# Kernel optimization log

Measured on AMD Instinct MI355X. Metric: run time of the kernel, lower is better.

Reference implementation:

```python
import jax, jax.numpy as jnp
import numpy as np

EPS_NORM = 1e-12
EPS_ENT = 1e-12
TEMPERATURE = 0.5
CONTRAST_DENOM = 128.0 * 100.0


def _l2_normalize(x, axis=-1):
    n = jnp.linalg.norm(x, axis=axis, keepdims=True)
    return x / jnp.maximum(n, EPS_NORM)


def setup_inputs() -> dict:
    key0 = jax.random.key(0)
    k1, k2, k3, k4 = jax.random.split(key0, 4)
    B, L, C = 16, 2048, 512
    M = 512
    return {
        "key": jax.random.normal(k1, (B, L, C), dtype=jnp.float32),
        "query": jax.random.normal(k2, (B, L, C), dtype=jnp.float32),
        "keys": jax.random.uniform(k3, (M, C), dtype=jnp.float32),
        "values": jax.random.uniform(k4, (M, C), dtype=jnp.float32),
        "mode": 0,
    }


def reference(key, query, keys, values, mode):
    B, L, C = key.shape
    k = _l2_normalize(key.reshape(-1, C))    # [T, C]
    q = _l2_normalize(query.reshape(-1, C))  # [T, C]

    # --- gatheringLoss ---
    score = jnp.einsum('tc,mc->tm', k, keys)            # [T, M]
    # top-1 of softmax(score) == argmax(score) (softmax is monotone)
    idx = jnp.argmax(score, axis=1)                     # [T]
    nearest_values = values[idx]                        # [T, C]
    gathering_loss = jnp.mean((q - nearest_values) ** 2)

    logits = score / TEMPERATURE                        # [T, M]
    logp = jax.nn.log_softmax(logits, axis=-1)
    gathered = jnp.take_along_axis(logp, idx[:, None], axis=1)  # [T, 1]
    contrast_loss = jnp.sum(gathered) / (-CONTRAST_DENOM)

    # --- read ---
    weights = jax.nn.softmax(score, axis=-1)            # [T, M]
    # EntropyLoss: mean over rows of -sum(w * log(w + eps))
    entropy_loss = jnp.mean(-jnp.sum(weights * jnp.log(weights + EPS_ENT), axis=-1))
    read_query = weights @ values                       # [T, C]

    return (read_query.reshape(B, L, C), entropy_loss, gathering_loss,
            contrast_loss, keys, values)
```

## Files before the change

### kernel.cpp

```cpp
#include <hip/hip_runtime.h>

typedef short short8 __attribute__((ext_vector_type(8)));
typedef float floatx4 __attribute__((ext_vector_type(4)));

#define T_ROWS 32768
#define C_DIM 512
#define M_DIM 512

__device__ __forceinline__ unsigned short f2bf(float f) {
    unsigned u = __builtin_bit_cast(unsigned, f);
    u = u + 0x7fffu + ((u >> 16) & 1u);
    return (unsigned short)(u >> 16);
}

__global__ __launch_bounds__(256) void pack_kernel(
    const float* __restrict__ keys, const float* __restrict__ values,
    unsigned short* __restrict__ keysFrag, unsigned short* __restrict__ valsFrag) {
    int tid = blockIdx.x * 256 + threadIdx.x;
    int e  = tid & 32767;
    int l  = e & 63;
    int NT = (e >> 6) & 31;
    int kt = e >> 11;
    int li = l & 15, q4 = l >> 4;
    unsigned short tmp[8];
    if (tid < 32768) {
        const float* s = keys + (size_t)(NT * 16 + li) * C_DIM + kt * 32 + q4 * 8;
#pragma unroll
        for (int j = 0; j < 8; j++) tmp[j] = f2bf(s[j]);
        unsigned short* d = keysFrag + ((size_t)(kt * 32 + NT) * 64 + l) * 8;
        ushort4 a = make_ushort4(tmp[0], tmp[1], tmp[2], tmp[3]);
        ushort4 b = make_ushort4(tmp[4], tmp[5], tmp[6], tmp[7]);
        *(ushort4*)d = a;
        *(ushort4*)(d + 4) = b;
    } else {
#pragma unroll
        for (int j = 0; j < 8; j++)
            tmp[j] = f2bf(values[(size_t)(kt * 32 + q4 * 8 + j) * C_DIM + NT * 16 + li]);
        unsigned short* d = valsFrag + ((size_t)(kt * 32 + NT) * 64 + l) * 8;
        ushort4 a = make_ushort4(tmp[0], tmp[1], tmp[2], tmp[3]);
        ushort4 b = make_ushort4(tmp[4], tmp[5], tmp[6], tmp[7]);
        *(ushort4*)d = a;
        *(ushort4*)(d + 4) = b;
    }
}

__global__ __launch_bounds__(512) void fused_kernel(
    const float* __restrict__ key,
    const unsigned short* __restrict__ keysFrag,
    const unsigned short* __restrict__ valsFrag,
    float* __restrict__ outRQ,
    float* __restrict__ scal,
    int* __restrict__ idxOut) {
    __shared__ char kq[32 * 1040];
    __shared__ float stats[2][4][16][8];
    __shared__ float finals[32][2];

    const int tid = threadIdx.x;
    const int w  = tid >> 6;
    const int l  = tid & 63;
    const int li = l & 15;
    const int q4 = l >> 4;
    const int row0 = blockIdx.x << 5;

    {
        int r = (w << 2) + q4;
        const float4* src = (const float4*)(key + (size_t)(row0 + r) * C_DIM);
        float4 v[8];
        float ss = 0.f;
#pragma unroll
        for (int i = 0; i < 8; i++) {
            v[i] = src[i * 16 + li];
            ss += v[i].x * v[i].x + v[i].y * v[i].y + v[i].z * v[i].z + v[i].w * v[i].w;
        }
#pragma unroll
        for (int m = 1; m < 16; m <<= 1) ss += __shfl_xor(ss, m, 64);
        float inv = 1.0f / fmaxf(sqrtf(ss), 1e-12f);
        char* dstrow = kq + r * 1040;
#pragma unroll
        for (int i = 0; i < 8; i++) {
            ushort4 b = make_ushort4(f2bf(v[i].x * inv), f2bf(v[i].y * inv),
                                     f2bf(v[i].z * inv), f2bf(v[i].w * inv));
            *(ushort4*)(dstrow + i * 128 + li * 8) = b;
        }
    }
    __syncthreads();

    const int rg = w >> 2;
    const int mc = w & 3;
    floatx4 acc1[8];
#pragma unroll
    for (int i = 0; i < 8; i++) acc1[i] = (floatx4){0.f, 0.f, 0.f, 0.f};
    const short8* kf = (const short8*)keysFrag;
    for (int kt = 0; kt < 16; kt++) {
        short8 a = *(const short8*)(kq + (rg * 16 + li) * 1040 + kt * 64 + q4 * 16);
#pragma unroll
        for (int nt = 0; nt < 8; nt++) {
            short8 b = kf[(size_t)((kt * 32 + mc * 8 + nt) * 64 + l)];
            acc1[nt] = __builtin_amdgcn_mfma_f32_16x16x32_bf16(a, b, acc1[nt], 0, 0, 0);
        }
    }

#pragma unroll
    for (int reg = 0; reg < 4; reg++) {
        float m = acc1[0][reg];
        int bi = (mc * 8 + 0) * 16 + li;
#pragma unroll
        for (int nt = 1; nt < 8; nt++) {
            float s = acc1[nt][reg];
            if (s > m) { m = s; bi = (mc * 8 + nt) * 16 + li; }
        }
        float z1 = 0.f, e1 = 0.f, z2 = 0.f;
#pragma unroll
        for (int nt = 0; nt < 8; nt++) {
            float s = acc1[nt][reg];
            float p = __expf(s - m);
            z1 += p; e1 += p * s; z2 += p * p;
        }
#pragma unroll
        for (int msk = 1; msk < 16; msk <<= 1) {
            float mo  = __shfl_xor(m,  msk, 64);
            float z1o = __shfl_xor(z1, msk, 64);
            float e1o = __shfl_xor(e1, msk, 64);
            float z2o = __shfl_xor(z2, msk, 64);
            int   bio = __shfl_xor(bi, msk, 64);
            if (mo > m) {
                float sc = __expf(m - mo);
                z1 = z1 * sc + z1o; e1 = e1 * sc + e1o; z2 = z2 * sc * sc + z2o;
                m = mo; bi = bio;
            } else if (mo == m) {
                z1 += z1o; e1 += e1o; z2 += z2o; bi = min(bi, bio);
            } else {
                float sc = __expf(mo - m);
                z1 += z1o * sc; e1 += e1o * sc; z2 += z2o * sc * sc;
            }
        }
        if (li == 0) {
            float* st = stats[rg][mc][q4 * 4 + reg];
            st[0] = m; st[1] = z1; st[2] = e1; st[3] = z2;
            ((int*)st)[4] = bi;
        }
    }
    __syncthreads();

    if (tid < 32) {
        int r = tid;
        const float* st0 = stats[r >> 4][0][r & 15];
        float m = st0[0], z1 = st0[1], e1 = st0[2], z2 = st0[3];
        int bi = ((const int*)st0)[4];
#pragma unroll
        for (int p = 1; p < 4; p++) {
            const float* st = stats[r >> 4][p][r & 15];
            float mo = st[0], z1o = st[1], e1o = st[2], z2o = st[3];
            int bio = ((const int*)st)[4];
            if (mo > m) {
                float sc = __expf(m - mo);
                z1 = z1 * sc + z1o; e1 = e1 * sc + e1o; z2 = z2 * sc * sc + z2o;
                m = mo; bi = bio;
            } else if (mo == m) {
                z1 += z1o; e1 += e1o; z2 += z2o; bi = min(bi, bio);
            } else {
                float sc = __expf(mo - m);
                z1 += z1o * sc; e1 += e1o * sc; z2 += z2o * sc * sc;
            }
        }
        finals[r][0] = m;
        finals[r][1] = 1.0f / z1;
        idxOut[row0 + r] = bi;
        float ent = m + __logf(z1) - e1 / z1;
        float con = __logf(z2);
#pragma unroll
        for (int msk = 1; msk < 32; msk <<= 1) {
            ent += __shfl_xor(ent, msk, 64);
            con += __shfl_xor(con, msk, 64);
        }
        if (tid == 0) {
            atomicAdd(&scal[0], ent * (1.0f / 32768.0f));
            atomicAdd(&scal[2], con * (1.0f / 12800.0f));
        }
    }
    __syncthreads();

#pragma unroll
    for (int reg = 0; reg < 4; reg++) {
        int r = rg * 16 + q4 * 4 + reg;
        float m1 = finals[r][0];
#pragma unroll
        for (int nt = 0; nt < 8; nt++) {
            float p = __expf(acc1[nt][reg] - m1);
            int col = (mc * 8 + nt) * 16 + li;
            *(unsigned short*)(kq + r * 1040 + col * 2) = f2bf(p);
        }
    }
    __syncthreads();

    floatx4 acc2[2][4];
#pragma unroll
    for (int g = 0; g < 2; g++)
#pragma unroll
        for (int nt = 0; nt < 4; nt++) acc2[g][nt] = (floatx4){0.f, 0.f, 0.f, 0.f};
    const short8* vf = (const short8*)valsFrag;
    for (int kt = 0; kt < 16; kt++) {
        short8 a0 = *(const short8*)(kq + li * 1040 + kt * 64 + q4 * 16);
        short8 a1 = *(const short8*)(kq + (16 + li) * 1040 + kt * 64 + q4 * 16);
#pragma unroll
        for (int nt = 0; nt < 4; nt++) {
            short8 b = vf[(size_t)((kt * 32 + w * 4 + nt) * 64 + l)];
            acc2[0][nt] = __builtin_amdgcn_mfma_f32_16x16x32_bf16(a0, b, acc2[0][nt], 0, 0, 0);
            acc2[1][nt] = __builtin_amdgcn_mfma_f32_16x16x32_bf16(a1, b, acc2[1][nt], 0, 0, 0);
        }
    }

#pragma unroll
    for (int g = 0; g < 2; g++) {
#pragma unroll
        for (int reg = 0; reg < 4; reg++) {
            int r = g * 16 + q4 * 4 + reg;
            float iz = finals[r][1];
            float* orow = outRQ + (size_t)(row0 + r) * C_DIM + w * 64 + li;
#pragma unroll
            for (int nt = 0; nt < 4; nt++) orow[nt * 16] = acc2[g][nt][reg] * iz;
        }
    }
}

__global__ __launch_bounds__(256) void gather_kernel(
    const float* __restrict__ query, const float* __restrict__ values,
    const int* __restrict__ idx, float* __restrict__ slot) {
    __shared__ float red[4];
    const int tid = threadIdx.x, w = tid >> 6, l = tid & 63;
    float acc = 0.f;
#pragma unroll
    for (int rr = 0; rr < 8; rr++) {
        int t = (blockIdx.x << 5) + w * 8 + rr;
        const float4* qr = (const float4*)(query + (size_t)t * C_DIM);
        float4 a = qr[l * 2], b = qr[l * 2 + 1];
        float ss = a.x * a.x + a.y * a.y + a.z * a.z + a.w * a.w +
                   b.x * b.x + b.y * b.y + b.z * b.z + b.w * b.w;
#pragma unroll
        for (int m = 1; m < 64; m <<= 1) ss += __shfl_xor(ss, m, 64);
        float inv = 1.0f / fmaxf(sqrtf(ss), 1e-12f);
        const float4* vr = (const float4*)(values + (size_t)idx[t] * C_DIM);
        float4 va = vr[l * 2], vb = vr[l * 2 + 1];
        float d;
        d = a.x * inv - va.x; acc += d * d;
        d = a.y * inv - va.y; acc += d * d;
        d = a.z * inv - va.z; acc += d * d;
        d = a.w * inv - va.w; acc += d * d;
        d = b.x * inv - vb.x; acc += d * d;
        d = b.y * inv - vb.y; acc += d * d;
        d = b.z * inv - vb.z; acc += d * d;
        d = b.w * inv - vb.w; acc += d * d;
    }
#pragma unroll
    for (int m = 1; m < 64; m <<= 1) acc += __shfl_xor(acc, m, 64);
    if (l == 0) red[w] = acc;
    __syncthreads();
    if (tid == 0)
        atomicAdd(slot, (red[0] + red[1] + red[2] + red[3]) * (1.0f / (32768.0f * 512.0f)));
}

extern "C" void kernel_launch(void* const* d_in, const int* in_sizes, int n_in,
                              void* d_out, int out_size, void* d_ws, size_t ws_size,
                              hipStream_t stream) {
    (void)in_sizes; (void)n_in; (void)out_size; (void)ws_size;
    const float* key    = (const float*)d_in[0];
    const float* query  = (const float*)d_in[1];
    const float* keysIn = (const float*)d_in[2];
    const float* valsIn = (const float*)d_in[3];
    float* out = (float*)d_out;

    unsigned short* keysFrag = (unsigned short*)d_ws;
    unsigned short* valsFrag = keysFrag + 512 * 512;
    int* idxBuf = (int*)(valsFrag + 512 * 512);

    float* outRQ   = out;
    float* scal    = out + 16777216;
    float* keysOut = out + 16777219;
    float* valsOut = keysOut + 262144;

    hipMemsetAsync(scal, 0, 3 * sizeof(float), stream);
    hipMemcpyAsync(keysOut, keysIn, 262144 * sizeof(float), hipMemcpyDeviceToDevice, stream);
    hipMemcpyAsync(valsOut, valsIn, 262144 * sizeof(float), hipMemcpyDeviceToDevice, stream);

    pack_kernel<<<256, 256, 0, stream>>>(keysIn, valsIn, keysFrag, valsFrag);
    fused_kernel<<<1024, 512, 0, stream>>>(key, keysFrag, valsFrag, outRQ, scal, idxBuf);
    gather_kernel<<<1024, 256, 0, stream>>>(query, valsIn, idxBuf, scal + 1);
}
```

Measured before the change: 279.4 us.

## Process 64 rows per block, prefetch B fragments, fuse gather loss into main kernel

New measurement: 246.2 us. -11.9%, faster.

```diff
diff --git a/kernel.cpp b/kernel.cpp
--- a/kernel.cpp
+++ b/kernel.cpp
@@ -3,9 +3,8 @@
 typedef short short8 __attribute__((ext_vector_type(8)));
 typedef float floatx4 __attribute__((ext_vector_type(4)));
 
-#define T_ROWS 32768
 #define C_DIM 512
-#define M_DIM 512
+#define KQ_STRIDE 1040
 
 __device__ __forceinline__ unsigned short f2bf(float f) {
     unsigned u = __builtin_bit_cast(unsigned, f);
@@ -28,42 +27,42 @@
 #pragma unroll
         for (int j = 0; j < 8; j++) tmp[j] = f2bf(s[j]);
         unsigned short* d = keysFrag + ((size_t)(kt * 32 + NT) * 64 + l) * 8;
-        ushort4 a = make_ushort4(tmp[0], tmp[1], tmp[2], tmp[3]);
-        ushort4 b = make_ushort4(tmp[4], tmp[5], tmp[6], tmp[7]);
-        *(ushort4*)d = a;
-        *(ushort4*)(d + 4) = b;
+        *(ushort4*)d       = make_ushort4(tmp[0], tmp[1], tmp[2], tmp[3]);
+        *(ushort4*)(d + 4) = make_ushort4(tmp[4], tmp[5], tmp[6], tmp[7]);
     } else {
 #pragma unroll
         for (int j = 0; j < 8; j++)
             tmp[j] = f2bf(values[(size_t)(kt * 32 + q4 * 8 + j) * C_DIM + NT * 16 + li]);
         unsigned short* d = valsFrag + ((size_t)(kt * 32 + NT) * 64 + l) * 8;
-        ushort4 a = make_ushort4(tmp[0], tmp[1], tmp[2], tmp[3]);
-        ushort4 b = make_ushort4(tmp[4], tmp[5], tmp[6], tmp[7]);
-        *(ushort4*)d = a;
-        *(ushort4*)(d + 4) = b;
+        *(ushort4*)d       = make_ushort4(tmp[0], tmp[1], tmp[2], tmp[3]);
+        *(ushort4*)(d + 4) = make_ushort4(tmp[4], tmp[5], tmp[6], tmp[7]);
     }
 }
 
-__global__ __launch_bounds__(512) void fused_kernel(
+__global__ __launch_bounds__(512, 4) void fused_kernel(
     const float* __restrict__ key,
+    const float* __restrict__ query,
     const unsigned short* __restrict__ keysFrag,
     const unsigned short* __restrict__ valsFrag,
+    const float* __restrict__ values,
     float* __restrict__ outRQ,
-    float* __restrict__ scal,
-    int* __restrict__ idxOut) {
-    __shared__ char kq[32 * 1040];
-    __shared__ float stats[2][4][16][8];
-    __shared__ float finals[32][2];
+    float* __restrict__ scal) {
+    __shared__ char kq[64 * KQ_STRIDE];
+    __shared__ float stats[8][64][6];
+    __shared__ float finals[64][2];
+    __shared__ int   idxsh[64];
+    __shared__ float gpart[8];
 
     const int tid = threadIdx.x;
     const int w  = tid >> 6;
     const int l  = tid & 63;
     const int li = l & 15;
     const int q4 = l >> 4;
-    const int row0 = blockIdx.x << 5;
-
-    {
-        int r = (w << 2) + q4;
+    const int row0 = blockIdx.x << 6;
+
+#pragma unroll
+    for (int it = 0; it < 2; it++) {
+        int r = (w << 3) + (it << 2) + q4;
         const float4* src = (const float4*)(key + (size_t)(row0 + r) * C_DIM);
         float4 v[8];
         float ss = 0.f;
@@ -75,7 +74,7 @@
 #pragma unroll
         for (int m = 1; m < 16; m <<= 1) ss += __shfl_xor(ss, m, 64);
         float inv = 1.0f / fmaxf(sqrtf(ss), 1e-12f);
-        char* dstrow = kq + r * 1040;
+        char* dstrow = kq + r * KQ_STRIDE;
 #pragma unroll
         for (int i = 0; i < 8; i++) {
             ushort4 b = make_ushort4(f2bf(v[i].x * inv), f2bf(v[i].y * inv),
@@ -85,71 +84,88 @@
     }
     __syncthreads();
 
-    const int rg = w >> 2;
-    const int mc = w & 3;
-    floatx4 acc1[8];
-#pragma unroll
-    for (int i = 0; i < 8; i++) acc1[i] = (floatx4){0.f, 0.f, 0.f, 0.f};
-    const short8* kf = (const short8*)keysFrag;
-    for (int kt = 0; kt < 16; kt++) {
-        short8 a = *(const short8*)(kq + (rg * 16 + li) * 1040 + kt * 64 + q4 * 16);
-#pragma unroll
-        for (int nt = 0; nt < 8; nt++) {
-            short8 b = kf[(size_t)((kt * 32 + mc * 8 + nt) * 64 + l)];
-            acc1[nt] = __builtin_amdgcn_mfma_f32_16x16x32_bf16(a, b, acc1[nt], 0, 0, 0);
-        }
-    }
-
-#pragma unroll
-    for (int reg = 0; reg < 4; reg++) {
-        float m = acc1[0][reg];
-        int bi = (mc * 8 + 0) * 16 + li;
-#pragma unroll
-        for (int nt = 1; nt < 8; nt++) {
-            float s = acc1[nt][reg];
-            if (s > m) { m = s; bi = (mc * 8 + nt) * 16 + li; }
-        }
-        float z1 = 0.f, e1 = 0.f, z2 = 0.f;
-#pragma unroll
-        for (int nt = 0; nt < 8; nt++) {
-            float s = acc1[nt][reg];
-            float p = __expf(s - m);
-            z1 += p; e1 += p * s; z2 += p * p;
-        }
-#pragma unroll
-        for (int msk = 1; msk < 16; msk <<= 1) {
-            float mo  = __shfl_xor(m,  msk, 64);
-            float z1o = __shfl_xor(z1, msk, 64);
-            float e1o = __shfl_xor(e1, msk, 64);
-            float z2o = __shfl_xor(z2, msk, 64);
-            int   bio = __shfl_xor(bi, msk, 64);
-            if (mo > m) {
-                float sc = __expf(m - mo);
-                z1 = z1 * sc + z1o; e1 = e1 * sc + e1o; z2 = z2 * sc * sc + z2o;
-                m = mo; bi = bio;
-            } else if (mo == m) {
-                z1 += z1o; e1 += e1o; z2 += z2o; bi = min(bi, bio);
-            } else {
-                float sc = __expf(mo - m);
-                z1 += z1o * sc; e1 += e1o * sc; z2 += z2o * sc * sc;
-            }
-        }
-        if (li == 0) {
-            float* st = stats[rg][mc][q4 * 4 + reg];
-            st[0] = m; st[1] = z1; st[2] = e1; st[3] = z2;
-            ((int*)st)[4] = bi;
-        }
-    }
-    __syncthreads();
-
-    if (tid < 32) {
+    floatx4 acc1[16];
+#pragma unroll
+    for (int i = 0; i < 16; i++) acc1[i] = (floatx4){0.f, 0.f, 0.f, 0.f};
+    {
+        const short8* kf = (const short8*)keysFrag;
+        short8 bcur[4], bnxt[4];
+#pragma unroll
+        for (int nt = 0; nt < 4; nt++) bcur[nt] = kf[(size_t)((w * 4 + nt) * 64 + l)];
+        for (int kt = 0; kt < 16; kt++) {
+            if (kt < 15) {
+#pragma unroll
+                for (int nt = 0; nt < 4; nt++)
+                    bnxt[nt] = kf[(size_t)(((kt + 1) * 32 + w * 4 + nt) * 64 + l)];
+            }
+            short8 a[4];
+#pragma unroll
+            for (int rg = 0; rg < 4; rg++)
+                a[rg] = *(const short8*)(kq + (rg * 16 + li) * KQ_STRIDE + kt * 64 + q4 * 16);
+#pragma unroll
+            for (int rg = 0; rg < 4; rg++)
+#pragma unroll
+                for (int nt = 0; nt < 4; nt++)
+                    acc1[rg * 4 + nt] = __builtin_amdgcn_mfma_f32_16x16x32_bf16(
+                        a[rg], bcur[nt], acc1[rg * 4 + nt], 0, 0, 0);
+#pragma unroll
+            for (int nt = 0; nt < 4; nt++) bcur[nt] = bnxt[nt];
+        }
+    }
+
+#pragma unroll
+    for (int rg = 0; rg < 4; rg++) {
+#pragma unroll
+        for (int reg = 0; reg < 4; reg++) {
+            float m = acc1[rg * 4][reg];
+            int bi = w * 64 + li;
+#pragma unroll
+            for (int nt = 1; nt < 4; nt++) {
+                float s = acc1[rg * 4 + nt][reg];
+                if (s > m) { m = s; bi = w * 64 + nt * 16 + li; }
+            }
+            float z1 = 0.f, e1 = 0.f, z2 = 0.f;
+#pragma unroll
+            for (int nt = 0; nt < 4; nt++) {
+                float s = acc1[rg * 4 + nt][reg];
+                float p = __expf(s - m);
+                z1 += p; e1 += p * s; z2 += p * p;
+            }
+#pragma unroll
+            for (int msk = 1; msk < 16; msk <<= 1) {
+                float mo  = __shfl_xor(m,  msk, 64);
+                float z1o = __shfl_xor(z1, msk, 64);
+                float e1o = __shfl_xor(e1, msk, 64);
+                float z2o = __shfl_xor(z2, msk, 64);
+                int   bio = __shfl_xor(bi, msk, 64);
+                if (mo > m) {
+                    float sc = __expf(m - mo);
+                    z1 = z1 * sc + z1o; e1 = e1 * sc + e1o; z2 = z2 * sc * sc + z2o;
+                    m = mo; bi = bio;
+                } else if (mo == m) {
+                    z1 += z1o; e1 += e1o; z2 += z2o; bi = min(bi, bio);
+                } else {
+                    float sc = __expf(mo - m);
+                    z1 += z1o * sc; e1 += e1o * sc; z2 += z2o * sc * sc;
+                }
+            }
+            if (li == 0) {
+                float* st = stats[w][rg * 16 + q4 * 4 + reg];
+                st[0] = m; st[1] = z1; st[2] = e1; st[3] = z2;
+                ((int*)st)[4] = bi;
+            }
+        }
+    }
+    __syncthreads();
+
+    if (tid < 64) {
         int r = tid;
-        const float* st0 = stats[r >> 4][0][r & 15];
+        const float* st0 = stats[0][r];
         float m = st0[0], z1 = st0[1], e1 = st0[2], z2 = st0[3];
         int bi = ((const int*)st0)[4];
 #pragma unroll
-        for (int p = 1; p < 4; p++) {
-            const float* st = stats[r >> 4][p][r & 15];
+        for (int p = 1; p < 8; p++) {
+            const float* st = stats[p][r];
             float mo = st[0], z1o = st[1], e1o = st[2], z2o = st[3];
             int bio = ((const int*)st)[4];
             if (mo > m) {
@@ -165,11 +181,11 @@
         }
         finals[r][0] = m;
         finals[r][1] = 1.0f / z1;
-        idxOut[row0 + r] = bi;
+        idxsh[r] = bi;
         float ent = m + __logf(z1) - e1 / z1;
         float con = __logf(z2);
 #pragma unroll
-        for (int msk = 1; msk < 32; msk <<= 1) {
+        for (int msk = 1; msk < 64; msk <<= 1) {
             ent += __shfl_xor(ent, msk, 64);
             con += __shfl_xor(con, msk, 64);
         }
@@ -181,82 +197,95 @@
     __syncthreads();
 
 #pragma unroll
-    for (int reg = 0; reg < 4; reg++) {
-        int r = rg * 16 + q4 * 4 + reg;
-        float m1 = finals[r][0];
-#pragma unroll
-        for (int nt = 0; nt < 8; nt++) {
-            float p = __expf(acc1[nt][reg] - m1);
-            int col = (mc * 8 + nt) * 16 + li;
-            *(unsigned short*)(kq + r * 1040 + col * 2) = f2bf(p);
-        }
-    }
-    __syncthreads();
-
-    floatx4 acc2[2][4];
-#pragma unroll
-    for (int g = 0; g < 2; g++)
-#pragma unroll
-        for (int nt = 0; nt < 4; nt++) acc2[g][nt] = (floatx4){0.f, 0.f, 0.f, 0.f};
-    const short8* vf = (const short8*)valsFrag;
-    for (int kt = 0; kt < 16; kt++) {
-        short8 a0 = *(const short8*)(kq + li * 1040 + kt * 64 + q4 * 16);
-        short8 a1 = *(const short8*)(kq + (16 + li) * 1040 + kt * 64 + q4 * 16);
-#pragma unroll
-        for (int nt = 0; nt < 4; nt++) {
-            short8 b = vf[(size_t)((kt * 32 + w * 4 + nt) * 64 + l)];
-            acc2[0][nt] = __builtin_amdgcn_mfma_f32_16x16x32_bf16(a0, b, acc2[0][nt], 0, 0, 0);
-            acc2[1][nt] = __builtin_amdgcn_mfma_f32_16x16x32_bf16(a1, b, acc2[1][nt], 0, 0, 0);
-        }
-    }
-
-#pragma unroll
-    for (int g = 0; g < 2; g++) {
+    for (int rg = 0; rg < 4; rg++) {
 #pragma unroll
         for (int reg = 0; reg < 4; reg++) {
-            int r = g * 16 + q4 * 4 + reg;
+            int r = rg * 16 + q4 * 4 + reg;
+            float m1 = finals[r][0];
+#pragma unroll
+            for (int nt = 0; nt < 4; nt++) {
+                float p = __expf(acc1[rg * 4 + nt][reg] - m1);
+                int col = w * 64 + nt * 16 + li;
+                *(unsigned short*)(kq + r * KQ_STRIDE + col * 2) = f2bf(p);
+            }
+        }
+    }
+    __syncthreads();
+
+    floatx4 acc2[16];
+#pragma unroll
+    for (int i = 0; i < 16; i++) acc2[i] = (floatx4){0.f, 0.f, 0.f, 0.f};
+    {
+        const short8* vf = (const short8*)valsFrag;
+        short8 bcur[4], bnxt[4];
+#pragma unroll
+        for (int nt = 0; nt < 4; nt++) bcur[nt] = vf[(size_t)((w * 4 + nt) * 64 + l)];
+        for (int kt = 0; kt < 16; kt++) {
+            if (kt < 15) {
+#pragma unroll
+                for (int nt = 0; nt < 4; nt++)
+                    bnxt[nt] = vf[(size_t)(((kt + 1) * 32 + w * 4 + nt) * 64 + l)];
+            }
+            short8 a[4];
+#pragma unroll
+            for (int rg = 0; rg < 4; rg++)
+                a[rg] = *(const short8*)(kq + (rg * 16 + li) * KQ_STRIDE + kt * 64 + q4 * 16);
+#pragma unroll
+            for (int rg = 0; rg < 4; rg++)
+#pragma unroll
+                for (int nt = 0; nt < 4; nt++)
+                    acc2[rg * 4 + nt] = __builtin_amdgcn_mfma_f32_16x16x32_bf16(
+                        a[rg], bcur[nt], acc2[rg * 4 + nt], 0, 0, 0);
+#pragma unroll
+            for (int nt = 0; nt < 4; nt++) bcur[nt] = bnxt[nt];
+        }
+    }
+
+#pragma unroll
+    for (int rg = 0; rg < 4; rg++) {
+#pragma unroll
+        for (int reg = 0; reg < 4; reg++) {
+            int r = rg * 16 + q4 * 4 + reg;
             float iz = finals[r][1];
             float* orow = outRQ + (size_t)(row0 + r) * C_DIM + w * 64 + li;
 #pragma unroll
-            for (int nt = 0; nt < 4; nt++) orow[nt * 16] = acc2[g][nt][reg] * iz;
-        }
-    }
-}
-
-__global__ __launch_bounds__(256) void gather_kernel(
-    const float* __restrict__ query, const float* __restrict__ values,
-    const int* __restrict__ idx, float* __restrict__ slot) {
-    __shared__ float red[4];
-    const int tid = threadIdx.x, w = tid >> 6, l = tid & 63;
-    float acc = 0.f;
+            for (int nt = 0; nt < 4; nt++) orow[nt * 16] = acc2[rg * 4 + nt][reg] * iz;
+        }
+    }
+
+    float gacc = 0.f;
 #pragma unroll
     for (int rr = 0; rr < 8; rr++) {
-        int t = (blockIdx.x << 5) + w * 8 + rr;
-        const float4* qr = (const float4*)(query + (size_t)t * C_DIM);
+        int r = (w << 3) + rr;
+        const float4* qr = (const float4*)(query + (size_t)(row0 + r) * C_DIM);
         float4 a = qr[l * 2], b = qr[l * 2 + 1];
         float ss = a.x * a.x + a.y * a.y + a.z * a.z + a.w * a.w +
                    b.x * b.x + b.y * b.y + b.z * b.z + b.w * b.w;
 #pragma unroll
         for (int m = 1; m < 64; m <<= 1) ss += __shfl_xor(ss, m, 64);
         float inv = 1.0f / fmaxf(sqrtf(ss), 1e-12f);
-        const float4* vr = (const float4*)(values + (size_t)idx[t] * C_DIM);
+        const float4* vr = (const float4*)(values + (size_t)idxsh[r] * C_DIM);
         float4 va = vr[l * 2], vb = vr[l * 2 + 1];
         float d;
-        d = a.x * inv - va.x; acc += d * d;
-        d = a.y * inv - va.y; acc += d * d;
-        d = a.z * inv - va.z; acc += d * d;
-        d = a.w * inv - va.w; acc += d * d;
-        d = b.x * inv - vb.x; acc += d * d;
-        d = b.y * inv - vb.y; acc += d * d;
-        d = b.z * inv - vb.z; acc += d * d;
-        d = b.w * inv - vb.w; acc += d * d;
-    }
-#pragma unroll
-    for (int m = 1; m < 64; m <<= 1) acc += __shfl_xor(acc, m, 64);
-    if (l == 0) red[w] = acc;
-    __syncthreads();
-    if (tid == 0)
-        atomicAdd(slot, (red[0] + red[1] + red[2] + red[3]) * (1.0f / (32768.0f * 512.0f)));
+        d = a.x * inv - va.x; gacc += d * d;
+        d = a.y * inv - va.y; gacc += d * d;
+        d = a.z * inv - va.z; gacc += d * d;
+        d = a.w * inv - va.w; gacc += d * d;
+        d = b.x * inv - vb.x; gacc += d * d;
+        d = b.y * inv - vb.y; gacc += d * d;
+        d = b.z * inv - vb.z; gacc += d * d;
+        d = b.w * inv - vb.w; gacc += d * d;
+    }
+#pragma unroll
+    for (int m = 1; m < 64; m <<= 1) gacc += __shfl_xor(gacc, m, 64);
+    if (l == 0) gpart[w] = gacc;
+    __syncthreads();
+    if (tid == 0) {
+        float s = 0.f;
+#pragma unroll
+        for (int i = 0; i < 8; i++) s += gpart[i];
+        atomicAdd(&scal[1], s * (1.0f / (32768.0f * 512.0f)));
+    }
 }
 
 extern "C" void kernel_launch(void* const* d_in, const int* in_sizes, int n_in,
@@ -271,7 +300,6 @@
 
     unsigned short* keysFrag = (unsigned short*)d_ws;
     unsigned short* valsFrag = keysFrag + 512 * 512;
-    int* idxBuf = (int*)(valsFrag + 512 * 512);
 
     float* outRQ   = out;
     float* scal    = out + 16777216;
@@ -283,6 +311,5 @@
     hipMemcpyAsync(valsOut, valsIn, 262144 * sizeof(float), hipMemcpyDeviceToDevice, stream);
 
     pack_kernel<<<256, 256, 0, stream>>>(keysIn, valsIn, keysFrag, valsFrag);
-    fused_kernel<<<1024, 512, 0, stream>>>(key, keysFrag, valsFrag, outRQ, scal, idxBuf);
-    gather_kernel<<<1024, 256, 0, stream>>>(query, valsIn, idxBuf, scal + 1);
+    fused_kernel<<<512, 512, 0, stream>>>(key, query, keysFrag, valsFrag, valsIn, outRQ, scal);
 }
```
